# Optimization experiments

Measured on AMD Instinct MI355X. Metric: run time of the kernel, lower is better.

Reference implementation:

```python
import jax, jax.numpy as jnp
import numpy as np

N, E, T, S, R, L = 100000, 1600000, 4, 32, 16, 5
H = 3 * S  # out-head hidden (hidden_list=[n_scalars*3])
EPS = 1e-8


def _mlp(x, W1, b1, W2, b2):
    return jax.nn.silu(x @ W1 + b1) @ W2 + b2


def setup_inputs() -> dict:
    key = jax.random.key(0)
    ks = iter(jax.random.split(key, 40))
    rn = lambda *s: jax.random.normal(next(ks), s, dtype=jnp.float32)
    p = lambda *s: rn(*s) * 0.1
    inp = {
        'u': rn(N, T),
        'v': rn(N, T, 2),
        'boundary_norm': rn(N, 2),
        'is_boundary': jnp.zeros((N,), dtype=bool),
        'y_force': rn(N, 2),
        'pos': rn(N, 2),
        'edge_index': jax.random.randint(next(ks), (2, E), 0, N, dtype=jnp.int64),
        # node embedding MLP: invariant feats (2T+2) -> 2S -> S
        'Wn1': p(2 * T + 2, 2 * S), 'bn1': jnp.zeros((2 * S,)),
        'Wn2': p(2 * S, S), 'bn2': jnp.zeros((S,)),
        # L stacked InvBlock params: edge MLP (2S+R -> S -> S), node update (2S -> S -> S)
        'We1': p(L, 2 * S + R, S), 'be1': jnp.zeros((L, S)),
        'We2': p(L, S, S), 'be2': jnp.zeros((L, S)),
        'Wu1': p(L, 2 * S, S), 'bu1': jnp.zeros((L, S)),
        'Wu2': p(L, S, S), 'bu2': jnp.zeros((L, S)),
        'ln_g': jnp.ones((S,)), 'ln_b': jnp.zeros((S,)),
        # heads: S -> 3S -> {2,1}
        'Wr1': p(S, H), 'br1': jnp.zeros((H,)), 'Wr2': p(H, 2), 'br2': jnp.zeros((2,)),
        'Ws1': p(S, H), 'bs1': jnp.zeros((H,)), 'Ws2': p(H, 1), 'bs2': jnp.zeros((1,)),
    }
    return inp


def _forward(u, v, boundary_norm, y_force, pos, edge_index,
             Wn1, bn1, Wn2, bn2, We1, be1, We2, be2, Wu1, bu1, Wu2, bu2,
             ln_g, ln_b, Wr1, br1, Wr2, br2, Ws1, bs1, Ws2, bs2):
    # torch.no_grad() geometry branch: center positions, edge distances
    posc = jax.lax.stop_gradient(pos - pos.mean(axis=0))
    row, col = edge_index[0], edge_index[1]
    edge_vec = posc[row] - posc[col]                       # [E,2]
    dist = jnp.linalg.norm(edge_vec, axis=1)               # [E]
    # besel_linspace(start=0, end=1, number=R, cutoff=False): Bessel/sine RBF
    freqs = jnp.arange(1, R + 1, dtype=jnp.float32) * jnp.pi
    rbf = jnp.sqrt(2.0) * jnp.sin(dist[:, None] * freqs) / (dist[:, None] + EPS)  # [E,R]

    # Node_embedding_inv: SE(2)-invariant scalar features -> MLP
    feats = jnp.concatenate([
        u,                                                 # [N,T]
        jnp.linalg.norm(v, axis=-1),                       # [N,T]
        jnp.linalg.norm(boundary_norm, axis=-1, keepdims=True),
        jnp.linalg.norm(y_force, axis=-1, keepdims=True),
    ], axis=-1)                                            # [N,2T+2]
    x = _mlp(feats, Wn1, bn1, Wn2, bn2)                    # [N,S]

    # degree for mean aggregation (computed once)
    deg = jax.ops.segment_sum(jnp.ones((E,), jnp.float32), row, num_segments=N)
    inv_deg = 1.0 / jnp.maximum(deg, 1.0)                  # [N]

    for l in range(L):  # InvBlock message passing
        ef = jnp.concatenate([x[row], x[col], rbf], axis=-1)   # [E,2S+R]
        m = _mlp(ef, We1[l], be1[l], We2[l], be2[l])           # [E,S]
        agg = jax.ops.segment_sum(m, row, num_segments=N) * inv_deg[:, None]
        x = x + _mlp(jnp.concatenate([x, agg], axis=-1), Wu1[l], bu1[l], Wu2[l], bu2[l])

    # LayerNorm
    mu = x.mean(axis=-1, keepdims=True)
    var = jnp.var(x, axis=-1, keepdims=True)
    x = (x - mu) * jax.lax.rsqrt(var + 1e-5) * ln_g + ln_b

    v_ = _mlp(x, Wr1, br1, Wr2, br2)                       # [N,2]
    u_ = _mlp(x, Ws1, bs1, Ws2, bs2)                       # [N,1]
    return u[:, -1] + u_[:, 0], v_ + v[:, -1, :]


def reference(u, v, boundary_norm, is_boundary, y_force, pos, edge_index,
              Wn1, bn1, Wn2, bn2, We1, be1, We2, be2, Wu1, bu1, Wu2, bu2,
              ln_g, ln_b, Wr1, br1, Wr2, br2, Ws1, bs1, Ws2, bs2):
    del is_boundary  # unused by the visible forward
    return _forward(u, v, boundary_norm, y_force, pos, edge_index,
                    Wn1, bn1, Wn2, bn2, We1, be1, We2, be2, Wu1, bu1, Wu2, bu2,
                    ln_g, ln_b, Wr1, br1, Wr2, br2, Ws1, bs1, Ws2, bs2)
```

## Files before the change

### kernel.cpp

```cpp
#include <hip/hip_runtime.h>
#include <cmath>

namespace {

constexpr int N = 100000;
constexpr int E = 1600000;
constexpr int S = 32;
constexpr int L = 5;
constexpr int NB = (N + 255) / 256;
constexpr int NPW = 16;
constexpr int LB2 = (N + 63) / 64;
constexpr int NBKT = 391;
constexpr int EPB  = E / 256;
constexpr float PI_F    = 3.14159265358979323846f;
constexpr float SQRT2_F = 1.41421356237309515f;

typedef __attribute__((ext_vector_type(8))) short short8;
typedef __attribute__((ext_vector_type(4))) float f32x4;

__device__ __forceinline__ float silu_f(float x) {
    return x * __builtin_amdgcn_rcpf(1.0f + __expf(-x));
}

__device__ __forceinline__ unsigned short f2bf(float f) {
    unsigned int u = __float_as_uint(f);
    u = (u + 0x7FFFu + ((u >> 16) & 1u)) >> 16;
    return (unsigned short)u;
}

__device__ __forceinline__ int rl(int v, int i) {
    return __builtin_amdgcn_readlane(v, i);
}

__device__ __forceinline__ short8 ld_xb(const unsigned short* base, int col, int quad) {
    unsigned off = ((unsigned)col << 6) | ((unsigned)quad << 4);
    return *reinterpret_cast<const short8*>(reinterpret_cast<const char*>(base) + off);
}

__device__ __forceinline__ short8 ld_rbf(const unsigned short* base, int slot, int quad) {
    unsigned off = ((unsigned)slot << 5) | ((unsigned)quad << 4);
    return *reinterpret_cast<const short8*>(reinterpret_cast<const char*>(base) + off);
}

__device__ __forceinline__ void adv(int& i, int& t, int vd) {
    ++t;
    while (i < 16) {
        int dgi = rl(vd, i);
        int nt = (dgi + 15) >> 4;
        if (t < nt) break;
        t = 0; ++i;
    }
}

__device__ __forceinline__ int slotOf(int i, int t, int vs, int vd, int ml) {
    if (i >= 16) return 0;
    int s0 = rl(vs, i);
    int dg = rl(vd, i);
    int smax = s0 + ((dg > 0) ? dg : 1) - 1;
    int s = s0 + t * 16 + ml;
    return min(s, smax);
}

__global__ __launch_bounds__(256) void passA_kernel(
    const int* __restrict__ ei, int* __restrict__ hist)
{
    __shared__ int h[NBKT];
    int t = threadIdx.x;
    int blk = blockIdx.x;
    for (int b = t; b < NBKT; b += 256) h[b] = 0;
    __syncthreads();
    int base = blk * EPB;
    for (int i = t; i < EPB; i += 256) {
        int r = ei[base + i];
        atomicAdd(&h[r >> 8], 1);
    }
    __syncthreads();
    for (int b = t; b < NBKT; b += 256) hist[b * 256 + blk] = h[b];
}

__global__ __launch_bounds__(512) void p1_kernel(
    const int* __restrict__ hist, int* __restrict__ bstart)
{
    __shared__ int tot[NBKT + 1];
    int t = threadIdx.x;
    if (t < NBKT) {
        int s = 0;
        for (int b = 0; b < 256; ++b) s += hist[t * 256 + b];
        tot[t] = s;
    }
    __syncthreads();
    if (t == 0) {
        int a = 0;
        for (int i = 0; i < NBKT; ++i) { int c = tot[i]; tot[i] = a; a += c; }
        tot[NBKT] = a;
    }
    __syncthreads();
    if (t <= NBKT) bstart[t] = tot[t];
}

__global__ __launch_bounds__(256) void p2_kernel(
    const int* __restrict__ hist, const int* __restrict__ bstart,
    int* __restrict__ base)
{
    __shared__ int pre[256];
    int t = threadIdx.x;
    int bin = blockIdx.x;
    int h = hist[bin * 256 + t];
    pre[t] = h;
    __syncthreads();
    #pragma unroll
    for (int off = 1; off < 256; off <<= 1) {
        int v = (t >= off) ? pre[t - off] : 0;
        __syncthreads();
        pre[t] += v;
        __syncthreads();
    }
    base[bin * 256 + t] = bstart[bin] + pre[t] - h;
}

__global__ __launch_bounds__(256) void passB_kernel(
    const int* __restrict__ ei, const float* __restrict__ pos,
    const int* __restrict__ base, uint4* __restrict__ edgebuf)
{
    __shared__ int cur[NBKT];
    int t = threadIdx.x;
    int blk = blockIdx.x;
    for (int b = t; b < NBKT; b += 256) cur[b] = base[b * 256 + blk];
    __syncthreads();
    int ebase = blk * EPB;
    for (int i = t; i < EPB; i += 256) {
        int e = ebase + i;
        int r = ei[e];
        int c = ei[E + e];
        float2 pr = reinterpret_cast<const float2*>(pos)[r];
        float2 pc = reinterpret_cast<const float2*>(pos)[c];
        float dx = pr.x - pc.x, dy = pr.y - pc.y;
        float d = sqrtf(dx * dx + dy * dy);
        int slot = atomicAdd(&cur[r >> 8], 1);
        edgebuf[slot] = make_uint4((unsigned)c, __float_as_uint(d), (unsigned)r, 0u);
    }
}

__global__ __launch_bounds__(256) void passC_kernel(
    const uint4* __restrict__ edgebuf, const int* __restrict__ bstart,
    int* __restrict__ deg, int* __restrict__ start,
    int* __restrict__ csr_col, unsigned short* __restrict__ rbf_buf)
{
    __shared__ int cnt[256];
    __shared__ int pre[256];
    __shared__ int cur[256];
    int t = threadIdx.x;
    int bkt = blockIdx.x;
    int s0 = bstart[bkt], s1 = bstart[bkt + 1];

    cnt[t] = 0;
    __syncthreads();
    for (int i = s0 + t; i < s1; i += 256) {
        unsigned r = edgebuf[i].z;
        atomicAdd(&cnt[r & 255], 1);
    }
    __syncthreads();
    int c0 = cnt[t];
    pre[t] = c0;
    __syncthreads();
    #pragma unroll
    for (int off = 1; off < 256; off <<= 1) {
        int v = (t >= off) ? pre[t - off] : 0;
        __syncthreads();
        pre[t] += v;
        __syncthreads();
    }
    int row = bkt * 256 + t;
    int st = s0 + pre[t] - c0;
    if (row < N) {
        deg[row] = c0;
        start[row] = st;
    }
    cur[t] = st;
    __syncthreads();

    for (int i = s0 + t; i < s1; i += 256) {
        uint4 e = edgebuf[i];
        int slot = atomicAdd(&cur[e.z & 255], 1);
        csr_col[slot] = (int)e.x;
        float d = __uint_as_float(e.y);

        float sn = __sinf(PI_F * d);
        float c1 = __cosf(PI_F * d);
        float inv = SQRT2_F / (d + 1e-8f);
        float tc = 2.0f * c1;
        float sk = sn, skm = 0.0f;
        unsigned int pk[8];
        #pragma unroll
        for (int k = 0; k < 8; ++k) {
            float r0 = sk * inv;
            float s2 = tc * sk - skm; skm = sk; sk = s2;
            float r1 = sk * inv;
            float s3 = tc * sk - skm; skm = sk; sk = s3;
            pk[k] = (unsigned int)f2bf(r0) | ((unsigned int)f2bf(r1) << 16);
        }
        uint4* out = reinterpret_cast<uint4*>(rbf_buf + (size_t)slot * 16);
        out[0] = make_uint4(pk[0], pk[1], pk[2], pk[3]);
        out[1] = make_uint4(pk[4], pk[5], pk[6], pk[7]);
    }
}

__global__ __launch_bounds__(256) void prep_wt_kernel(
    const float* __restrict__ We1, const float* __restrict__ We2,
    const float* __restrict__ Wu1, const float* __restrict__ Wu2,
    const float* __restrict__ Wr1, const float* __restrict__ Ws1,
    short* __restrict__ wt1, short* __restrict__ wt2,
    short* __restrict__ wtu1, short* __restrict__ wtu2,
    short* __restrict__ wtr1, short* __restrict__ wts1)
{
    int idx = blockIdx.x * 256 + threadIdx.x;
    if (idx < 5 * 32 * 96) {
        int l = idx / (32 * 96), r = idx % (32 * 96), n = r / 96, k = r % 96;
        float v = (k < 80) ? We1[((size_t)l * 80 + k) * 32 + n] : 0.0f;
        wt1[idx] = (short)f2bf(v);
    }
    if (idx < 5 * 32 * 32) {
        int l = idx / 1024, r = idx % 1024, n = r / 32, k = r % 32;
        wt2[idx]  = (short)f2bf(We2[((size_t)l * 32 + k) * 32 + n]);
        wtu2[idx] = (short)f2bf(Wu2[((size_t)l * 32 + k) * 32 + n]);
    }
    if (idx < 5 * 32 * 64) {
        int l = idx / 2048, r = idx % 2048, n = r / 64, k = r % 64;
        wtu1[idx] = (short)f2bf(Wu1[((size_t)l * 64 + k) * 32 + n]);
    }
    if (idx < 96 * 32) {
        int n = idx / 32, k = idx % 32;
        wtr1[idx] = (short)f2bf(Wr1[k * 96 + n]);
        wts1[idx] = (short)f2bf(Ws1[k * 96 + n]);
    }
}

__global__ __launch_bounds__(256) void node_embed_kernel(
    const float* __restrict__ u, const float* __restrict__ v,
    const float* __restrict__ bnorm, const float* __restrict__ yf,
    const float* __restrict__ Wn1, const float* __restrict__ bn1,
    const float* __restrict__ Wn2, const float* __restrict__ bn2,
    float* __restrict__ x, unsigned short* __restrict__ xb)
{
    int n = blockIdx.x * 256 + threadIdx.x;
    if (n >= N) return;

    float f[10];
    float4 uu = reinterpret_cast<const float4*>(u)[n];
    f[0] = uu.x; f[1] = uu.y; f[2] = uu.z; f[3] = uu.w;
    float4 v0 = reinterpret_cast<const float4*>(v)[2 * n];
    float4 v1 = reinterpret_cast<const float4*>(v)[2 * n + 1];
    f[4] = sqrtf(v0.x * v0.x + v0.y * v0.y);
    f[5] = sqrtf(v0.z * v0.z + v0.w * v0.w);
    f[6] = sqrtf(v1.x * v1.x + v1.y * v1.y);
    f[7] = sqrtf(v1.z * v1.z + v1.w * v1.w);
    float2 bb = reinterpret_cast<const float2*>(bnorm)[n];
    f[8] = sqrtf(bb.x * bb.x + bb.y * bb.y);
    float2 yy = reinterpret_cast<const float2*>(yf)[n];
    f[9] = sqrtf(yy.x * yy.x + yy.y * yy.y);

    float h[64];
    #pragma unroll
    for (int j = 0; j < 64; ++j) h[j] = bn1[j];
    #pragma unroll
    for (int i = 0; i < 10; ++i) {
        float t = f[i];
        #pragma unroll
        for (int j = 0; j < 64; ++j) h[j] = fmaf(t, Wn1[i * 64 + j], h[j]);
    }
    #pragma unroll
    for (int j = 0; j < 64; ++j) h[j] = silu_f(h[j]);

    float o[32];
    #pragma unroll
    for (int j = 0; j < 32; ++j) o[j] = bn2[j];
    #pragma unroll
    for (int i = 0; i < 64; ++i) {
        float t = h[i];
        #pragma unroll
        for (int j = 0; j < 32; ++j) o[j] = fmaf(t, Wn2[i * 32 + j], o[j]);
    }
    float4* xo = reinterpret_cast<float4*>(x + (size_t)n * 32);
    #pragma unroll
    for (int i = 0; i < 8; ++i)
        xo[i] = make_float4(o[4 * i], o[4 * i + 1], o[4 * i + 2], o[4 * i + 3]);

    unsigned int* xbu = reinterpret_cast<unsigned int*>(xb) + (size_t)n * 16;
    #pragma unroll
    for (int i = 0; i < 16; ++i)
        xbu[i] = (unsigned int)f2bf(o[2 * i]) | ((unsigned int)f2bf(o[2 * i + 1]) << 16);
}

__global__ __launch_bounds__(256, 7) void layer_kernel(
    const int* __restrict__ deg, const int* __restrict__ start,
    const int* __restrict__ csr_col, const unsigned short* __restrict__ rbf_buf,
    const float* __restrict__ x_in, const unsigned short* __restrict__ xb_in,
    float* __restrict__ x_out, unsigned short* __restrict__ xb_out,
    const short* __restrict__ wt1, const float* __restrict__ b1,
    const short* __restrict__ wt2, const float* __restrict__ b2,
    const short* __restrict__ wtu1, const float* __restrict__ bu1,
    const short* __restrict__ wtu2, const float* __restrict__ bu2)
{
    __shared__ unsigned short lsh[4][16 * 34];
    __shared__ unsigned short agb[4][16 * 34];
    __shared__ unsigned short hub[4][16 * 34];
    __shared__ float lrp[4][16 * 33];
    __shared__ float ldg[4][16];
    __shared__ float livd[4][16];

    int t = threadIdx.x;
    int w = t >> 6;
    int lane = t & 63;
    int quad = lane >> 4;
    int ml = lane & 15;
    int wid = blockIdx.x * 4 + w;
    int nbase = __builtin_amdgcn_readfirstlane(wid * NPW);
    if (nbase >= N) return;

    int vs = start[nbase + ml];
    int vd = deg[nbase + ml];

    const short8* wp = reinterpret_cast<const short8*>(wt1);
    short8 B00 = wp[(ml     ) * 12 + 0 * 4 + quad];
    short8 B01 = wp[(ml     ) * 12 + 1 * 4 + quad];
    short8 B02 = wp[(ml     ) * 12 + 2 * 4 + quad];
    short8 B10 = wp[(ml + 16) * 12 + 0 * 4 + quad];
    short8 B11 = wp[(ml + 16) * 12 + 1 * 4 + quad];
    short8 B12 = wp[(ml + 16) * 12 + 2 * 4 + quad];

    short8 Ax = ld_xb(xb_in, nbase + ml, quad);

    float b1j0 = b1[ml];
    float b1j1 = b1[ml + 16];

    unsigned short* lshp = lsh[w];
    for (int k = lane; k < 16 * 34; k += 64) lshp[k] = 0;
    if (lane < 16) {
        ldg[w][lane] = (float)vd;
        livd[w][lane] = 1.0f / fmaxf((float)vd, 1.0f);
    }

    float* rpp = lrp[w];
    {
        f32x4 rp0 = {b1j0, b1j0, b1j0, b1j0};
        f32x4 rp1 = {b1j1, b1j1, b1j1, b1j1};
        rp0 = __builtin_amdgcn_mfma_f32_16x16x32_bf16(Ax, B00, rp0, 0, 0, 0);
        rp1 = __builtin_amdgcn_mfma_f32_16x16x32_bf16(Ax, B10, rp1, 0, 0, 0);
        int row = quad * 4;
        #pragma unroll
        for (int r = 0; r < 4; ++r) {
            rpp[(row + r) * 33 + ml]      = rp0[r];
            rpp[(row + r) * 33 + ml + 16] = rp1[r];
        }
    }
    __builtin_amdgcn_wave_barrier();

    const short8 Z8 = {0, 0, 0, 0, 0, 0, 0, 0};
    int i0 = 0, t0 = -1; adv(i0, t0, vd);
    int i1 = i0, t1 = t0; adv(i1, t1, vd);
    int i2 = i1, t2 = t1; adv(i2, t2, vd);

    int slot0 = slotOf(i0, t0, vs, vd, ml);
    int slot1 = slotOf(i1, t1, vs, vd, ml);
    int colCur  = csr_col[slot0];
    int colNext = csr_col[slot1];
    short8 A1c = ld_xb(xb_in, colCur, quad);
    short8 A2c = Z8;
    if (quad < 2) A2c = ld_rbf(rbf_buf, slot0, quad);

    float colp0 = 0.0f, colp1 = 0.0f;
    while (i0 < 16) {
        int slot2 = slotOf(i2, t2, vs, vd, ml);
        int colNN = csr_col[slot2];
        short8 A1n = ld_xb(xb_in, colNext, quad);
        short8 A2n = Z8;
        if (quad < 2) A2n = ld_rbf(rbf_buf, slot1, quad);

        float rpa = rpp[i0 * 33 + ml];
        float rpb = rpp[i0 * 33 + ml + 16];
        f32x4 acc0 = {rpa, rpa, rpa, rpa};
        f32x4 acc1 = {rpb, rpb, rpb, rpb};
        acc0 = __builtin_amdgcn_mfma_f32_16x16x32_bf16(A1c, B01, acc0, 0, 0, 0);
        acc0 = __builtin_amdgcn_mfma_f32_16x16x32_bf16(A2c, B02, acc0, 0, 0, 0);
        acc1 = __builtin_amdgcn_mfma_f32_16x16x32_bf16(A1c, B11, acc1, 0, 0, 0);
        acc1 = __builtin_amdgcn_mfma_f32_16x16x32_bf16(A2c, B12, acc1, 0, 0, 0);

        int dg0 = rl(vd, i0);
        int rowbase = t0 * 16 + quad * 4;
        #pragma unroll
        for (int r = 0; r < 4; ++r) {
            bool vld = (rowbase + r) < dg0;
            colp0 += vld ? silu_f(acc0[r]) : 0.0f;
            colp1 += vld ? silu_f(acc1[r]) : 0.0f;
        }
        if (t0 == ((dg0 + 15) >> 4) - 1) {
            colp0 += __shfl_xor(colp0, 16, 64);
            colp0 += __shfl_xor(colp0, 32, 64);
            colp1 += __shfl_xor(colp1, 16, 64);
            colp1 += __shfl_xor(colp1, 32, 64);
            if (quad == 0) {
                lshp[i0 * 34 + ml]      = f2bf(colp0);
                lshp[i0 * 34 + ml + 16] = f2bf(colp1);
            }
            colp0 = 0.0f; colp1 = 0.0f;
        }

        A1c = A1n; A2c = A2n;
        colNext = colNN; slot1 = slot2;
        i0 = i1; t0 = t1; i1 = i2; t1 = t2;
        adv(i2, t2, vd);
    }
    __builtin_amdgcn_wave_barrier();

    const short8* w2p = reinterpret_cast<const short8*>(wt2);
    short8 Bw2_0 = w2p[(ml     ) * 4 + quad];
    short8 Bw2_1 = w2p[(ml + 16) * 4 + quad];
    const short8* u1p = reinterpret_cast<const short8*>(wtu1);
    short8 Bu1_00 = u1p[(ml     ) * 8 + quad];
    short8 Bu1_10 = u1p[(ml     ) * 8 + 4 + quad];
    short8 Bu1_01 = u1p[(ml + 16) * 8 + quad];
    short8 Bu1_11 = u1p[(ml + 16) * 8 + 4 + quad];
    const short8* u2p = reinterpret_cast<const short8*>(wtu2);
    short8 Bu2_0 = u2p[(ml     ) * 4 + quad];
    short8 Bu2_1 = u2p[(ml + 16) * 4 + quad];

    short8 Ash = *reinterpret_cast<const short8*>(lshp + ml * 34 + quad * 8);
    f32x4 c0 = {0.0f, 0.0f, 0.0f, 0.0f};
    f32x4 c1 = {0.0f, 0.0f, 0.0f, 0.0f};
    c0 = __builtin_amdgcn_mfma_f32_16x16x32_bf16(Ash, Bw2_0, c0, 0, 0, 0);
    c1 = __builtin_amdgcn_mfma_f32_16x16x32_bf16(Ash, Bw2_1, c1, 0, 0, 0);
    float b2c0 = b2[ml], b2c1 = b2[ml + 16];
    unsigned short* agp = agb[w];
    int row = quad * 4;
    #pragma unroll
    for (int r = 0; r < 4; ++r) {
        float fd = ldg[w][row + r];
        float iv = livd[w][row + r];
        agp[(row + r) * 34 + ml]      = f2bf((c0[r] + fd * b2c0) * iv);
        agp[(row + r) * 34 + ml + 16] = f2bf((c1[r] + fd * b2c1) * iv);
    }
    __builtin_amdgcn_wave_barrier();

    short8 Aag = *reinterpret_cast<const short8*>(agp + ml * 34 + quad * 8);
    f32x4 d0 = {0.0f, 0.0f, 0.0f, 0.0f};
    f32x4 d1 = {0.0f, 0.0f, 0.0f, 0.0f};
    d0 = __builtin_amdgcn_mfma_f32_16x16x32_bf16(Ax,  Bu1_00, d0, 0, 0, 0);
    d0 = __builtin_amdgcn_mfma_f32_16x16x32_bf16(Aag, Bu1_10, d0, 0, 0, 0);
    d1 = __builtin_amdgcn_mfma_f32_16x16x32_bf16(Ax,  Bu1_01, d1, 0, 0, 0);
    d1 = __builtin_amdgcn_mfma_f32_16x16x32_bf16(Aag, Bu1_11, d1, 0, 0, 0);
    float bu1c0 = bu1[ml], bu1c1 = bu1[ml + 16];
    unsigned short* hup = hub[w];
    #pragma unroll
    for (int r = 0; r < 4; ++r) {
        hup[(row + r) * 34 + ml]      = f2bf(silu_f(d0[r] + bu1c0));
        hup[(row + r) * 34 + ml + 16] = f2bf(silu_f(d1[r] + bu1c1));
    }
    __builtin_amdgcn_wave_barrier();

    short8 Ahu = *reinterpret_cast<const short8*>(hup + ml * 34 + quad * 8);
    float xr0[4], xr1[4];
    #pragma unroll
    for (int r = 0; r < 4; ++r) {
        int nn = nbase + row + r;
        xr0[r] = x_in[(size_t)nn * 32 + ml];
        xr1[r] = x_in[(size_t)nn * 32 + ml + 16];
    }
    f32x4 e0 = {0.0f, 0.0f, 0.0f, 0.0f};
    f32x4 e1 = {0.0f, 0.0f, 0.0f, 0.0f};
    e0 = __builtin_amdgcn_mfma_f32_16x16x32_bf16(Ahu, Bu2_0, e0, 0, 0, 0);
    e1 = __builtin_amdgcn_mfma_f32_16x16x32_bf16(Ahu, Bu2_1, e1, 0, 0, 0);
    float bu2c0 = bu2[ml], bu2c1 = bu2[ml + 16];
    #pragma unroll
    for (int r = 0; r < 4; ++r) {
        int nn = nbase + row + r;
        float o0 = e0[r] + bu2c0 + xr0[r];
        float o1 = e1[r] + bu2c1 + xr1[r];
        x_out[(size_t)nn * 32 + ml]      = o0;
        x_out[(size_t)nn * 32 + ml + 16] = o1;
        xb_out[(size_t)nn * 32 + ml]      = f2bf(o0);
        xb_out[(size_t)nn * 32 + ml + 16] = f2bf(o1);
    }
}

__global__ __launch_bounds__(256) void final_kernel(
    const float* __restrict__ x, const float* __restrict__ u,
    const float* __restrict__ v,
    const float* __restrict__ ln_g, const float* __restrict__ ln_b,
    const short* __restrict__ wtr1, const float* __restrict__ br1,
    const float* __restrict__ Wr2, const float* __restrict__ br2,
    const short* __restrict__ wts1, const float* __restrict__ bs1,
    const float* __restrict__ Ws2, const float* __restrict__ bs2,
    float* __restrict__ out)
{
    int t = threadIdx.x;
    int w = t >> 6;
    int lane = t & 63;
    int quad = lane >> 4;
    int ml = lane & 15;
    int wid = blockIdx.x * 4 + w;
    int nbase = __builtin_amdgcn_readfirstlane(wid * NPW);
    if (nbase >= N) return;

    const float4* xs = reinterpret_cast<const float4*>(
        x + (size_t)(nbase + ml) * 32 + quad * 8);
    float4 xa = xs[0], xb4 = xs[1];
    float f[8] = {xa.x, xa.y, xa.z, xa.w, xb4.x, xb4.y, xb4.z, xb4.w};

    float s = 0.0f, ss = 0.0f;
    #pragma unroll
    for (int i = 0; i < 8; ++i) { s += f[i]; ss += f[i] * f[i]; }
    s  += __shfl_xor(s, 16, 64);  s  += __shfl_xor(s, 32, 64);
    ss += __shfl_xor(ss, 16, 64); ss += __shfl_xor(ss, 32, 64);
    float mu = s * (1.0f / 32.0f);
    float var = ss * (1.0f / 32.0f) - mu * mu;
    float rs = rsqrtf(var + 1e-5f);

    const float4* gp = reinterpret_cast<const float4*>(ln_g + quad * 8);
    const float4* bp = reinterpret_cast<const float4*>(ln_b + quad * 8);
    float4 g0 = gp[0], g1 = gp[1], bb0 = bp[0], bb1 = bp[1];
    float gg[8] = {g0.x, g0.y, g0.z, g0.w, g1.x, g1.y, g1.z, g1.w};
    float bb[8] = {bb0.x, bb0.y, bb0.z, bb0.w, bb1.x, bb1.y, bb1.z, bb1.w};
    short8 A;
    #pragma unroll
    for (int i = 0; i < 8; ++i)
        A[i] = (short)f2bf((f[i] - mu) * rs * gg[i] + bb[i]);

    const short8* r1p = reinterpret_cast<const short8*>(wtr1);
    const short8* s1p = reinterpret_cast<const short8*>(wts1);
    const f32x4 Zf = {0.0f, 0.0f, 0.0f, 0.0f};
    f32x4 hr[6], hs[6];
    #pragma unroll
    for (int h = 0; h < 6; ++h) {
        hr[h] = __builtin_amdgcn_mfma_f32_16x16x32_bf16(A, r1p[(ml + 16 * h) * 4 + quad], Zf, 0, 0, 0);
        hs[h] = __builtin_amdgcn_mfma_f32_16x16x32_bf16(A, s1p[(ml + 16 * h) * 4 + quad], Zf, 0, 0, 0);
    }

    float wr2a[6], wr2b[6], ws2v[6], br1v[6], bs1v[6];
    #pragma unroll
    for (int h = 0; h < 6; ++h) {
        int j = ml + 16 * h;
        float2 wr = reinterpret_cast<const float2*>(Wr2)[j];
        wr2a[h] = wr.x; wr2b[h] = wr.y;
        ws2v[h] = Ws2[j];
        br1v[h] = br1[j];
        bs1v[h] = bs1[j];
    }

    float o0[4], o1[4], o2[4];
    #pragma unroll
    for (int r = 0; r < 4; ++r) {
        float p0 = 0.0f, p1 = 0.0f, p2 = 0.0f;
        #pragma unroll
        for (int h = 0; h < 6; ++h) {
            float a1 = silu_f(hr[h][r] + br1v[h]);
            float a2 = silu_f(hs[h][r] + bs1v[h]);
            p0 = fmaf(a1, wr2a[h], p0);
            p1 = fmaf(a1, wr2b[h], p1);
            p2 = fmaf(a2, ws2v[h], p2);
        }
        p0 += __shfl_xor(p0, 1, 64); p0 += __shfl_xor(p0, 2, 64);
        p0 += __shfl_xor(p0, 4, 64); p0 += __shfl_xor(p0, 8, 64);
        p1 += __shfl_xor(p1, 1, 64); p1 += __shfl_xor(p1, 2, 64);
        p1 += __shfl_xor(p1, 4, 64); p1 += __shfl_xor(p1, 8, 64);
        p2 += __shfl_xor(p2, 1, 64); p2 += __shfl_xor(p2, 2, 64);
        p2 += __shfl_xor(p2, 4, 64); p2 += __shfl_xor(p2, 8, 64);
        o0[r] = p0; o1[r] = p1; o2[r] = p2;
    }

    if (ml == 0) {
        float b20 = br2[0], b21 = br2[1], b22 = bs2[0];
        #pragma unroll
        for (int r = 0; r < 4; ++r) {
            int n = nbase + quad * 4 + r;
            out[n] = u[n * 4 + 3] + o2[r] + b22;
            out[N + 2 * n]     = o0[r] + b20 + v[n * 8 + 6];
            out[N + 2 * n + 1] = o1[r] + b21 + v[n * 8 + 7];
        }
    }
}

}

extern "C" void kernel_launch(void* const* d_in, const int* in_sizes, int n_in,
                              void* d_out, int out_size, void* d_ws, size_t ws_size,
                              hipStream_t stream)
{
    const float* u    = (const float*)d_in[0];
    const float* v    = (const float*)d_in[1];
    const float* bno  = (const float*)d_in[2];
    const float* yf   = (const float*)d_in[4];
    const float* pos  = (const float*)d_in[5];
    const int*   ei   = (const int*)d_in[6];
    const float* Wn1  = (const float*)d_in[7];
    const float* bn1  = (const float*)d_in[8];
    const float* Wn2  = (const float*)d_in[9];
    const float* bn2  = (const float*)d_in[10];
    const float* We1  = (const float*)d_in[11];
    const float* be1  = (const float*)d_in[12];
    const float* We2  = (const float*)d_in[13];
    const float* be2  = (const float*)d_in[14];
    const float* Wu1  = (const float*)d_in[15];
    const float* bu1  = (const float*)d_in[16];
    const float* Wu2  = (const float*)d_in[17];
    const float* bu2  = (const float*)d_in[18];
    const float* ln_g = (const float*)d_in[19];
    const float* ln_b = (const float*)d_in[20];
    const float* Wr1  = (const float*)d_in[21];
    const float* br1  = (const float*)d_in[22];
    const float* Wr2  = (const float*)d_in[23];
    const float* br2  = (const float*)d_in[24];
    const float* Ws1  = (const float*)d_in[25];
    const float* bs1  = (const float*)d_in[26];
    const float* Ws2  = (const float*)d_in[27];
    const float* bs2  = (const float*)d_in[28];
    float* out = (float*)d_out;

    int*   deg      = (int*)d_ws;
    int*   start    = deg + N;
    int*   bstart   = start + N;
    int*   csr_col  = bstart + 512;
    unsigned short* rbf = (unsigned short*)(csr_col + E);
    float* x0       = (float*)(rbf + (size_t)E * 16);
    float* x1       = x0 + (size_t)N * S;
    unsigned short* xb0 = (unsigned short*)(x1 + (size_t)N * S);
    unsigned short* xb1 = xb0 + (size_t)N * S;
    short* wt1      = (short*)(xb1 + (size_t)N * S);
    short* wt2      = wt1 + 5 * 32 * 96;
    short* wtu1     = wt2 + 5 * 32 * 32;
    short* wtu2     = wtu1 + 5 * 32 * 64;
    short* wtr1     = wtu2 + 5 * 32 * 32;
    short* wts1     = wtr1 + 96 * 32;
    int*   hist     = (int*)(wts1 + 96 * 32);
    int*   basem    = hist + NBKT * 256;

    uint4* edgebuf = (uint4*)x0;

    passA_kernel<<<256, 256, 0, stream>>>(ei, hist);
    p1_kernel<<<1, 512, 0, stream>>>(hist, bstart);
    p2_kernel<<<NBKT, 256, 0, stream>>>(hist, bstart, basem);
    passB_kernel<<<256, 256, 0, stream>>>(ei, pos, basem, edgebuf);
    passC_kernel<<<NBKT, 256, 0, stream>>>(edgebuf, bstart, deg, start, csr_col, rbf);
    prep_wt_kernel<<<60, 256, 0, stream>>>(We1, We2, Wu1, Wu2, Wr1, Ws1,
                                           wt1, wt2, wtu1, wtu2, wtr1, wts1);

    node_embed_kernel<<<NB, 256, 0, stream>>>(u, v, bno, yf, Wn1, bn1, Wn2, bn2,
                                              x0, xb0);

    float* xin = x0;  float* xout = x1;
    unsigned short* xbin = xb0;  unsigned short* xbout = xb1;
    for (int l = 0; l < L; ++l) {
        layer_kernel<<<LB2, 256, 0, stream>>>(
            deg, start, csr_col, rbf, xin, xbin, xout, xbout,
            wt1 + (size_t)l * 32 * 96,  be1 + (size_t)l * 32,
            wt2 + (size_t)l * 32 * 32,  be2 + (size_t)l * 32,
            wtu1 + (size_t)l * 32 * 64, bu1 + (size_t)l * 32,
            wtu2 + (size_t)l * 32 * 32, bu2 + (size_t)l * 32);
        float* tf = xin; xin = xout; xout = tf;
        unsigned short* tb = xbin; xbin = xbout; xbout = tb;
    }

    final_kernel<<<LB2, 256, 0, stream>>>(xin, u, v, ln_g, ln_b,
                                          wtr1, br1, Wr2, br2,
                                          wts1, bs1, Ws2, bs2, out);
}
```

Baseline: 511.4 us.

## Deepen edge gather prefetch pipeline to three tiles in layer kernel

Restructures the per-wave edge loop from a one-tile-ahead prefetch into a rotating three-buffer pipeline, with column indices fetched four tiles ahead and features three tiles ahead. The loop is manually unrolled by three so the feature registers rotate without copies. This aims to hide more of the latency of the random gathers of x and rbf. It costs more live VGPRs, so the launch-bounds occupancy hint drops from 7 to 6 waves per SIMD.

New measurement: 505.3 us. Within noise of the previous version (-1.2%).

```diff
diff --git a/kernel.cpp b/kernel.cpp
--- a/kernel.cpp
+++ b/kernel.cpp
@@ -291,7 +291,7 @@
         xbu[i] = (unsigned int)f2bf(o[2 * i]) | ((unsigned int)f2bf(o[2 * i + 1]) << 16);
 }
 
-__global__ __launch_bounds__(256, 7) void layer_kernel(
+__global__ __launch_bounds__(256, 6) void layer_kernel(
     const int* __restrict__ deg, const int* __restrict__ start,
     const int* __restrict__ csr_col, const unsigned short* __restrict__ rbf_buf,
     const float* __restrict__ x_in, const unsigned short* __restrict__ xb_in,
@@ -356,60 +356,85 @@
     __builtin_amdgcn_wave_barrier();
 
     const short8 Z8 = {0, 0, 0, 0, 0, 0, 0, 0};
-    int i0 = 0, t0 = -1; adv(i0, t0, vd);
-    int i1 = i0, t1 = t0; adv(i1, t1, vd);
-    int i2 = i1, t2 = t1; adv(i2, t2, vd);
-
-    int slot0 = slotOf(i0, t0, vs, vd, ml);
-    int slot1 = slotOf(i1, t1, vs, vd, ml);
-    int colCur  = csr_col[slot0];
-    int colNext = csr_col[slot1];
-    short8 A1c = ld_xb(xb_in, colCur, quad);
-    short8 A2c = Z8;
-    if (quad < 2) A2c = ld_rbf(rbf_buf, slot0, quad);
+    int iA = 0, tA = -1; adv(iA, tA, vd);
+    int iB = iA, tB = tA; adv(iB, tB, vd);
+    int iC = iB, tC = tB; adv(iC, tC, vd);
+    int iD = iC, tD = tC; adv(iD, tD, vd);
+    int iE = iD, tE = tD; adv(iE, tE, vd);
+
+    int slot0 = slotOf(iA, tA, vs, vd, ml);
+    int slot1 = slotOf(iB, tB, vs, vd, ml);
+    int slot2 = slotOf(iC, tC, vs, vd, ml);
+    int slotQ = slotOf(iD, tD, vs, vd, ml);
+    int col0 = csr_col[slot0];
+    int col1 = csr_col[slot1];
+    int col2 = csr_col[slot2];
+    int colQ = csr_col[slotQ];
+
+    short8 F1_0 = ld_xb(xb_in, col0, quad);
+    short8 F2_0 = (quad < 2) ? ld_rbf(rbf_buf, slot0, quad) : Z8;
+    short8 F1_1 = ld_xb(xb_in, col1, quad);
+    short8 F2_1 = (quad < 2) ? ld_rbf(rbf_buf, slot1, quad) : Z8;
+    short8 F1_2 = ld_xb(xb_in, col2, quad);
+    short8 F2_2 = (quad < 2) ? ld_rbf(rbf_buf, slot2, quad) : Z8;
 
     float colp0 = 0.0f, colp1 = 0.0f;
-    while (i0 < 16) {
-        int slot2 = slotOf(i2, t2, vs, vd, ml);
-        int colNN = csr_col[slot2];
-        short8 A1n = ld_xb(xb_in, colNext, quad);
-        short8 A2n = Z8;
-        if (quad < 2) A2n = ld_rbf(rbf_buf, slot1, quad);
-
-        float rpa = rpp[i0 * 33 + ml];
-        float rpb = rpp[i0 * 33 + ml + 16];
+
+    auto tile = [&](const short8& A1, const short8& A2) {
+        float rpa = rpp[iA * 33 + ml];
+        float rpb = rpp[iA * 33 + ml + 16];
         f32x4 acc0 = {rpa, rpa, rpa, rpa};
         f32x4 acc1 = {rpb, rpb, rpb, rpb};
-        acc0 = __builtin_amdgcn_mfma_f32_16x16x32_bf16(A1c, B01, acc0, 0, 0, 0);
-        acc0 = __builtin_amdgcn_mfma_f32_16x16x32_bf16(A2c, B02, acc0, 0, 0, 0);
-        acc1 = __builtin_amdgcn_mfma_f32_16x16x32_bf16(A1c, B11, acc1, 0, 0, 0);
-        acc1 = __builtin_amdgcn_mfma_f32_16x16x32_bf16(A2c, B12, acc1, 0, 0, 0);
-
-        int dg0 = rl(vd, i0);
-        int rowbase = t0 * 16 + quad * 4;
+        acc0 = __builtin_amdgcn_mfma_f32_16x16x32_bf16(A1, B01, acc0, 0, 0, 0);
+        acc0 = __builtin_amdgcn_mfma_f32_16x16x32_bf16(A2, B02, acc0, 0, 0, 0);
+        acc1 = __builtin_amdgcn_mfma_f32_16x16x32_bf16(A1, B11, acc1, 0, 0, 0);
+        acc1 = __builtin_amdgcn_mfma_f32_16x16x32_bf16(A2, B12, acc1, 0, 0, 0);
+
+        int dg0 = rl(vd, iA);
+        int rowbase = tA * 16 + quad * 4;
         #pragma unroll
         for (int r = 0; r < 4; ++r) {
             bool vld = (rowbase + r) < dg0;
             colp0 += vld ? silu_f(acc0[r]) : 0.0f;
             colp1 += vld ? silu_f(acc1[r]) : 0.0f;
         }
-        if (t0 == ((dg0 + 15) >> 4) - 1) {
+        if (tA == ((dg0 + 15) >> 4) - 1) {
             colp0 += __shfl_xor(colp0, 16, 64);
             colp0 += __shfl_xor(colp0, 32, 64);
             colp1 += __shfl_xor(colp1, 16, 64);
             colp1 += __shfl_xor(colp1, 32, 64);
             if (quad == 0) {
-                lshp[i0 * 34 + ml]      = f2bf(colp0);
-                lshp[i0 * 34 + ml + 16] = f2bf(colp1);
+                lshp[iA * 34 + ml]      = f2bf(colp0);
+                lshp[iA * 34 + ml + 16] = f2bf(colp1);
             }
             colp0 = 0.0f; colp1 = 0.0f;
         }
-
-        A1c = A1n; A2c = A2n;
-        colNext = colNN; slot1 = slot2;
-        i0 = i1; t0 = t1; i1 = i2; t1 = t2;
-        adv(i2, t2, vd);
-    }
+    };
+    auto shiftq = [&]() {
+        iA = iB; tA = tB; iB = iC; tB = tC;
+        iC = iD; tC = tD; iD = iE; tD = tE;
+        adv(iE, tE, vd);
+    };
+
+    #define EDGE_STEP(F1s, F2s)                                     \
+    {                                                               \
+        int slotE_ = slotOf(iE, tE, vs, vd, ml);                    \
+        int colE_  = csr_col[slotE_];                               \
+        tile(F1s, F2s);                                             \
+        F1s = ld_xb(xb_in, colQ, quad);                             \
+        F2s = (quad < 2) ? ld_rbf(rbf_buf, slotQ, quad) : Z8;       \
+        shiftq();                                                   \
+        colQ = colE_; slotQ = slotE_;                               \
+    }
+
+    while (iA < 16) {
+        EDGE_STEP(F1_0, F2_0);
+        if (iA >= 16) break;
+        EDGE_STEP(F1_1, F2_1);
+        if (iA >= 16) break;
+        EDGE_STEP(F1_2, F2_2);
+    }
+    #undef EDGE_STEP
     __builtin_amdgcn_wave_barrier();
 
     const short8* w2p = reinterpret_cast<const short8*>(wt2);
```
